# Performance work log

Measured on AMD Instinct MI355X. Metric: run time of the kernel, lower is better.

Reference implementation:

```python
import jax, jax.numpy as jnp
import numpy as np

GROUP = 32
HEADS = 8
EPS = 1e-5


def setup_inputs() -> dict:
    key = jax.random.key(0)
    k1, k2, k3 = jax.random.split(key, 3)
    C = 512
    x = jax.random.normal(k1, (8, C, 32, 32), dtype=jnp.float32)
    gn_w = jnp.ones((C,), dtype=jnp.float32)
    gn_b = jnp.zeros((C,), dtype=jnp.float32)
    # 1x1 convs == channel matmuls; init like torch conv default (kaiming-ish scale)
    w_qkv = jax.random.normal(k2, (3 * C, C), dtype=jnp.float32) * (1.0 / np.sqrt(C))
    w_proj = jax.random.normal(k3, (C, C), dtype=jnp.float32) * (1.0 / np.sqrt(C))
    return {"x": x, "gn_w": gn_w, "gn_b": gn_b, "w_qkv": w_qkv, "w_proj": w_proj}


def _forward(x, gn_w, gn_b, w_qkv, w_proj):
    B, C, H, W = x.shape
    N = H * W
    d = C // HEADS
    scale = d ** -0.5
    # GroupNorm over (channels_per_group, H, W)
    xg = x.reshape(B, GROUP, C // GROUP, H, W)
    mean = xg.mean(axis=(2, 3, 4), keepdims=True)
    var = xg.var(axis=(2, 3, 4), keepdims=True)
    xn = ((xg - mean) * jax.lax.rsqrt(var + EPS)).reshape(B, C, H, W)
    xn = xn * gn_w[None, :, None, None] + gn_b[None, :, None, None]
    # 1x1 conv QKV: [3C, C] x [B, C, H, W]
    qkv = jnp.einsum('oc,bchw->bohw', w_qkv, xn)
    q, k, v = jnp.split(qkv, 3, axis=1)

    def to_heads(t):  # b (h d) H W -> b h N d
        return t.reshape(B, HEADS, d, N).transpose(0, 1, 3, 2)

    q, k, v = to_heads(q), to_heads(k), to_heads(v)
    scores = jnp.einsum('bhid,bhjd->bhij', q, k) * scale
    probs = jax.nn.softmax(scores, axis=-1)
    out = jnp.einsum('bhij,bhjd->bhid', probs, v)
    # b h N d -> b (h d) H W
    out = out.transpose(0, 1, 3, 2).reshape(B, C, H, W)
    out = jnp.einsum('oc,bchw->bohw', w_proj, out)
    return x + out


def reference(x, gn_w, gn_b, w_qkv, w_proj):
    return _forward(x, gn_w, gn_b, w_qkv, w_proj)
```

## Files before the change

kernel.cpp:

```cpp
#include <hip/hip_runtime.h>

typedef __attribute__((ext_vector_type(4))) float f32x4;
typedef __attribute__((ext_vector_type(8))) __bf16 bf16x8;
typedef __attribute__((ext_vector_type(8))) unsigned short ushort8;

#define BATCH 8
#define CH    512
#define NN    1024
#define GRP   32
#define NHEAD 8
#define DH    64
#define QBLK  128
#define KBLK  64

static constexpr size_t OFF_STATS = 0;
static constexpr size_t OFF_WQB   = 4096;
static constexpr size_t OFF_WPB   = OFF_WQB + (size_t)1536*512*2;
static constexpr size_t OFF_XNT   = OFF_WPB + (size_t)512*512*2;
static constexpr size_t OFF_QKB   = OFF_XNT + (size_t)BATCH*NN*CH*2;
static constexpr size_t OFF_VT    = OFF_QKB + (size_t)BATCH*NN*1024*2;
static constexpr size_t OFF_ATTNT = OFF_VT  + (size_t)BATCH*CH*NN*2;

static __device__ __forceinline__ unsigned short f2bf(float f){
  union { float f; unsigned u; } cv; cv.f = f;
  unsigned u = cv.u;
  u += 0x7fffu + ((u >> 16) & 1u);
  return (unsigned short)(u >> 16);
}

static __device__ __forceinline__ unsigned pack2bf(float lo, float hi){
  union { __bf16 h[2]; unsigned u; } v;
  v.h[0] = (__bf16)lo; v.h[1] = (__bf16)hi;
  return v.u;
}

static __device__ __forceinline__ void gload_lds16(const unsigned short* g, unsigned short* l){
  __builtin_amdgcn_global_load_lds((const __attribute__((address_space(1))) void*)g,
                                   (__attribute__((address_space(3))) void*)l, 16, 0, 0);
}

__global__ __launch_bounds__(256) void cvt_w_k(const float* __restrict__ wq, const float* __restrict__ wp,
                                               unsigned short* __restrict__ wqb, unsigned short* __restrict__ wpb){
  int i = blockIdx.x*256 + threadIdx.x;
  if (i < 1536*512) wqb[i] = f2bf(wq[i]);
  if (i < 512*512)  wpb[i] = f2bf(wp[i]);
}

__global__ __launch_bounds__(256) void gn_stats_k(const float* __restrict__ x, float* __restrict__ stats){
  int bg = blockIdx.x;
  const float4* base = (const float4*)(x + (size_t)bg * (16*NN));
  float s = 0.f, ss = 0.f;
  #pragma unroll 4
  for (int idx = threadIdx.x; idx < 16*NN/4; idx += 256){
    float4 v = base[idx];
    s  += (v.x + v.y) + (v.z + v.w);
    ss += (v.x*v.x + v.y*v.y) + (v.z*v.z + v.w*v.w);
  }
  for (int off = 32; off > 0; off >>= 1){ s += __shfl_down(s, off); ss += __shfl_down(ss, off); }
  __shared__ float red[8];
  int w = threadIdx.x >> 6, l = threadIdx.x & 63;
  if (l == 0){ red[w*2] = s; red[w*2+1] = ss; }
  __syncthreads();
  if (threadIdx.x == 0){
    float S  = red[0]+red[2]+red[4]+red[6];
    float SS = red[1]+red[3]+red[5]+red[7];
    float mean = S * (1.f/(16*NN));
    float var  = SS * (1.f/(16*NN)) - mean*mean;
    stats[bg*2]   = mean;
    stats[bg*2+1] = rsqrtf(var + 1e-5f);
  }
}

__global__ __launch_bounds__(256) void gn_apply_k(const float* __restrict__ x, const float* __restrict__ stats,
                                                  const float* __restrict__ gw, const float* __restrict__ gb,
                                                  unsigned short* __restrict__ xnT){
  int b = blockIdx.z, c0 = blockIdx.y*64, n0 = blockIdx.x*64;
  __shared__ unsigned short T[64][65];
  int t = threadIdx.x;
  int nl = t & 63;
  int cb = t >> 6;
  #pragma unroll
  for (int r = 0; r < 16; ++r){
    int cl = cb + r*4;
    int c  = c0 + cl;
    float xv   = x[((size_t)b*CH + c)*NN + n0 + nl];
    float mean = stats[(b*GRP + (c>>4))*2];
    float rstd = stats[(b*GRP + (c>>4))*2 + 1];
    float sc   = rstd * gw[c];
    T[cl][nl]  = f2bf((xv - mean)*sc + gb[c]);
  }
  __syncthreads();
  #pragma unroll
  for (int r = 0; r < 16; ++r){
    int nlocal = cb + r*4;
    xnT[((size_t)b*NN + n0 + nlocal)*CH + c0 + nl] = T[nl][nlocal];
  }
}

__global__ __launch_bounds__(256) void qkv_gemm_k(const unsigned short* __restrict__ wq,
                                                  const unsigned short* __restrict__ xnT,
                                                  unsigned short* __restrict__ qkb,
                                                  unsigned short* __restrict__ vT){
  int b  = blockIdx.z;
  int m0 = blockIdx.y * 128;
  int n0 = blockIdx.x * 128;
  __shared__ unsigned short As[128][64];
  __shared__ unsigned short Bs[128][64];
  int t = threadIdx.x;
  int w = t >> 6, l = t & 63;
  int wm = w >> 1, wn = w & 1;
  f32x4 acc[4][4] = {};
  const unsigned short* Ag = wq  + (size_t)(m0 + w*32)*512;
  const unsigned short* Bg = xnT + ((size_t)b*NN + n0 + w*32)*512;
  int r8 = l >> 3;
  int c8 = ((l & 7) ^ r8) * 8;
  int lr = l & 15, lg = l >> 4;
  int xr = (lr & 7) << 3;
  for (int k0 = 0; k0 < 512; k0 += 64){
    #pragma unroll
    for (int i = 0; i < 4; ++i){
      gload_lds16(Ag + (size_t)(i*8 + r8)*512 + k0 + c8, &As[w*32 + i*8][0]);
      gload_lds16(Bg + (size_t)(i*8 + r8)*512 + k0 + c8, &Bs[w*32 + i*8][0]);
    }
    __syncthreads();
    #pragma unroll
    for (int ks = 0; ks < 2; ++ks){
      bf16x8 af[4], bfr[4];
      #pragma unroll
      for (int mf = 0; mf < 4; ++mf) af[mf]  = *(const bf16x8*)&As[wm*64 + mf*16 + lr][(ks*32 + lg*8) ^ xr];
      #pragma unroll
      for (int nf = 0; nf < 4; ++nf) bfr[nf] = *(const bf16x8*)&Bs[wn*64 + nf*16 + lr][(ks*32 + lg*8) ^ xr];
      #pragma unroll
      for (int mf = 0; mf < 4; ++mf)
        #pragma unroll
        for (int nf = 0; nf < 4; ++nf)
          acc[mf][nf] = __builtin_amdgcn_mfma_f32_16x16x32_bf16(af[mf], bfr[nf], acc[mf][nf], 0, 0, 0);
    }
    __syncthreads();
  }
  int lq = l >> 4;
  float scl = (m0 < 512) ? 0.18033688f : 1.0f;
  if (m0 < 1024){
    #pragma unroll
    for (int mf = 0; mf < 4; ++mf)
      #pragma unroll
      for (int nf = 0; nf < 4; ++nf)
        #pragma unroll
        for (int r = 0; r < 4; ++r){
          int o = m0 + wm*64 + mf*16 + lq*4 + r;
          int n = n0 + wn*64 + nf*16 + lr;
          qkb[((size_t)b*NN + n)*1024 + o] = f2bf(acc[mf][nf][r] * scl);
        }
  } else {
    #pragma unroll
    for (int mf = 0; mf < 4; ++mf)
      #pragma unroll
      for (int nf = 0; nf < 4; ++nf)
        #pragma unroll
        for (int r = 0; r < 4; ++r){
          int o = m0 + wm*64 + mf*16 + lq*4 + r;
          int n = n0 + wn*64 + nf*16 + lr;
          vT[((size_t)b*512 + (o - 1024))*NN + n] = f2bf(acc[mf][nf][r]);
        }
  }
}

#define STAGE_KV(TT, BUF)                                                                \
  {                                                                                      \
    int jj = (TT) * KBLK;                                                                \
    _Pragma("unroll") for (int ch = 0; ch < 2; ++ch){                                    \
      gload_lds16(Kg + (size_t)(jj + w*16 + ch*8 + srow)*1024 + scol,                    \
                  &KV[0][BUF][w*16 + ch*8][0]);                                          \
      gload_lds16(Vg + (size_t)(w*16 + ch*8 + srow)*NN + jj + scol,                      \
                  &KV[1][BUF][w*16 + ch*8][0]);                                          \
    }                                                                                    \
  }

__global__ __launch_bounds__(256) void attn_k(const unsigned short* __restrict__ qkb,
                                              const unsigned short* __restrict__ vT,
                                              unsigned short* __restrict__ attnT){
  int bh = blockIdx.x;
  int b = bh >> 3, h = bh & 7;
  int q0 = blockIdx.y * QBLK;
  int t = threadIdx.x;
  int w = t >> 6, l = t & 63;
  int lr = l & 15, lg = l >> 4;

  __shared__ unsigned short KV[2][2][64][64];

  int srow = l >> 3;
  int scol = ((l & 7) ^ srow) * 8;
  const unsigned short* Kg = qkb + (size_t)b*NN*1024 + 512 + h*DH;
  const unsigned short* Vg = vT  + (size_t)(b*NHEAD + h)*DH*NN;

  bf16x8 qf[2][2];
  #pragma unroll
  for (int mf = 0; mf < 2; ++mf)
    #pragma unroll
    for (int ks = 0; ks < 2; ++ks){
      int row = q0 + w*32 + mf*16 + lr;
      qf[mf][ks] = *(const bf16x8*)(qkb + ((size_t)b*NN + row)*1024 + h*DH + ks*32 + lg*8);
    }

  float lsum[2] = {0.f, 0.f};
  f32x4 accO[2][4] = {};

  STAGE_KV(0, 0)
  __syncthreads();

  for (int tt = 0; tt < 16; ++tt){
    int cur = tt & 1;
    if (tt < 15) STAGE_KV(tt + 1, cur ^ 1)
    int xr = (lr & 7) * 8;
    bf16x8 kf[2][4], vf[2][4];
    #pragma unroll
    for (int ks = 0; ks < 2; ++ks)
      #pragma unroll
      for (int nf = 0; nf < 4; ++nf){
        kf[ks][nf] = *(const bf16x8*)&KV[0][cur][nf*16 + lr][(ks*32 + lg*8) ^ xr];
        vf[ks][nf] = *(const bf16x8*)&KV[1][cur][nf*16 + lr][(ks*32 + lg*8) ^ xr];
      }
    #pragma unroll
    for (int mf = 0; mf < 2; ++mf){
      f32x4 sT[4] = {};
      __builtin_amdgcn_s_setprio(1);
      #pragma unroll
      for (int ks = 0; ks < 2; ++ks)
        #pragma unroll
        for (int nf = 0; nf < 4; ++nf)
          sT[nf] = __builtin_amdgcn_mfma_f32_16x16x32_bf16(kf[ks][nf], qf[mf][ks], sT[nf], 0, 0, 0);
      __builtin_amdgcn_s_setprio(0);
      unsigned pk[4][2];
      #pragma unroll
      for (int nf = 0; nf < 4; ++nf){
        float p0 = exp2f(sT[nf][0]), p1 = exp2f(sT[nf][1]);
        float p2 = exp2f(sT[nf][2]), p3 = exp2f(sT[nf][3]);
        lsum[mf] += (p0 + p1) + (p2 + p3);
        pk[nf][0] = pack2bf(p0, p1);
        pk[nf][1] = pack2bf(p2, p3);
      }
      int srcA = lr + ((lg & 1) << 5);
      int srcB = srcA + 16;
      bool hsel = (lg >> 1) != 0;
      #pragma unroll
      for (int ks = 0; ks < 2; ++ks){
        unsigned a0 = (unsigned)__shfl((int)pk[2*ks  ][0], srcA);
        unsigned a1 = (unsigned)__shfl((int)pk[2*ks  ][1], srcA);
        unsigned a2 = (unsigned)__shfl((int)pk[2*ks  ][0], srcB);
        unsigned a3 = (unsigned)__shfl((int)pk[2*ks  ][1], srcB);
        unsigned b0 = (unsigned)__shfl((int)pk[2*ks+1][0], srcA);
        unsigned b1 = (unsigned)__shfl((int)pk[2*ks+1][1], srcA);
        unsigned b2 = (unsigned)__shfl((int)pk[2*ks+1][0], srcB);
        unsigned b3 = (unsigned)__shfl((int)pk[2*ks+1][1], srcB);
        union { unsigned u[4]; bf16x8 v; } pf;
        pf.u[0] = hsel ? b0 : a0;
        pf.u[1] = hsel ? b1 : a1;
        pf.u[2] = hsel ? b2 : a2;
        pf.u[3] = hsel ? b3 : a3;
        __builtin_amdgcn_s_setprio(1);
        #pragma unroll
        for (int nf = 0; nf < 4; ++nf)
          accO[mf][nf] = __builtin_amdgcn_mfma_f32_16x16x32_bf16(vf[ks][nf], pf.v, accO[mf][nf], 0, 0, 0);
        __builtin_amdgcn_s_setprio(0);
      }
    }
    __syncthreads();
  }

  #pragma unroll
  for (int mf = 0; mf < 2; ++mf){
    lsum[mf] += __shfl_xor(lsum[mf], 16);
    lsum[mf] += __shfl_xor(lsum[mf], 32);
    lsum[mf] = 1.f / lsum[mf];
  }

  unsigned short* Ob = &KV[0][0][0][0] + w * 2304;
  #pragma unroll
  for (int mf = 0; mf < 2; ++mf)
    #pragma unroll
    for (int nf = 0; nf < 4; ++nf)
      #pragma unroll
      for (int r = 0; r < 4; ++r){
        __bf16 hv = (__bf16)(accO[mf][nf][r] * lsum[mf]);
        Ob[mf*1152 + lr*72 + nf*16 + lg*4 + r] = *(unsigned short*)&hv;
      }
  __syncthreads();
  int qr = l >> 2, cc = (l & 3) * 16;
  #pragma unroll
  for (int mf = 0; mf < 2; ++mf){
    bf16x8 o0 = *(const bf16x8*)&Ob[mf*1152 + qr*72 + cc];
    bf16x8 o1 = *(const bf16x8*)&Ob[mf*1152 + qr*72 + cc + 8];
    unsigned short* dst = attnT + ((size_t)b*NN + q0 + w*32 + mf*16 + qr)*CH + h*DH + cc;
    *(bf16x8*)dst = o0;
    *(bf16x8*)(dst + 8) = o1;
  }
}

__global__ __launch_bounds__(256) void proj_gemm_k(const unsigned short* __restrict__ wp,
                                                   const unsigned short* __restrict__ attnT,
                                                   const float* __restrict__ x, float* __restrict__ out){
  int b  = blockIdx.z;
  int m0 = blockIdx.y * 64;
  int n0 = blockIdx.x * 128;
  __shared__ unsigned short As[64][64];
  __shared__ unsigned short Bs[128][64];
  int t = threadIdx.x;
  int w = t >> 6, l = t & 63;
  int wm = w >> 1, wn = w & 1;
  f32x4 acc[2][4] = {};
  const unsigned short* Ag = wp    + (size_t)(m0 + w*16)*512;
  const unsigned short* Bg = attnT + ((size_t)b*NN + n0 + w*32)*512;
  int r8 = l >> 3;
  int c8 = ((l & 7) ^ r8) * 8;
  int lr = l & 15, lg = l >> 4;
  int xr = (lr & 7) << 3;
  for (int k0 = 0; k0 < 512; k0 += 64){
    #pragma unroll
    for (int i = 0; i < 2; ++i)
      gload_lds16(Ag + (size_t)(i*8 + r8)*512 + k0 + c8, &As[w*16 + i*8][0]);
    #pragma unroll
    for (int i = 0; i < 4; ++i)
      gload_lds16(Bg + (size_t)(i*8 + r8)*512 + k0 + c8, &Bs[w*32 + i*8][0]);
    __syncthreads();
    #pragma unroll
    for (int ks = 0; ks < 2; ++ks){
      bf16x8 af[2], bfr[4];
      #pragma unroll
      for (int mf = 0; mf < 2; ++mf) af[mf]  = *(const bf16x8*)&As[wm*32 + mf*16 + lr][(ks*32 + lg*8) ^ xr];
      #pragma unroll
      for (int nf = 0; nf < 4; ++nf) bfr[nf] = *(const bf16x8*)&Bs[wn*64 + nf*16 + lr][(ks*32 + lg*8) ^ xr];
      #pragma unroll
      for (int mf = 0; mf < 2; ++mf)
        #pragma unroll
        for (int nf = 0; nf < 4; ++nf)
          acc[mf][nf] = __builtin_amdgcn_mfma_f32_16x16x32_bf16(af[mf], bfr[nf], acc[mf][nf], 0, 0, 0);
    }
    __syncthreads();
  }
  int lq = l >> 4;
  #pragma unroll
  for (int mf = 0; mf < 2; ++mf)
    #pragma unroll
    for (int nf = 0; nf < 4; ++nf)
      #pragma unroll
      for (int r = 0; r < 4; ++r){
        int o = m0 + wm*32 + mf*16 + lq*4 + r;
        int n = n0 + wn*64 + nf*16 + lr;
        size_t idx = ((size_t)b*CH + o)*NN + n;
        out[idx] = x[idx] + acc[mf][nf][r];
      }
}

extern "C" void kernel_launch(void* const* d_in, const int* in_sizes, int n_in,
                              void* d_out, int out_size, void* d_ws, size_t ws_size,
                              hipStream_t stream){
  const float* x  = (const float*)d_in[0];
  const float* gw = (const float*)d_in[1];
  const float* gb = (const float*)d_in[2];
  const float* wq = (const float*)d_in[3];
  const float* wp = (const float*)d_in[4];
  float* out = (float*)d_out;
  char* ws = (char*)d_ws;
  float*          stats = (float*)(ws + OFF_STATS);
  unsigned short* wqb   = (unsigned short*)(ws + OFF_WQB);
  unsigned short* wpb   = (unsigned short*)(ws + OFF_WPB);
  unsigned short* xnT   = (unsigned short*)(ws + OFF_XNT);
  unsigned short* qkb   = (unsigned short*)(ws + OFF_QKB);
  unsigned short* vT    = (unsigned short*)(ws + OFF_VT);
  unsigned short* attnT = (unsigned short*)(ws + OFF_ATTNT);

  hipLaunchKernelGGL(cvt_w_k,    dim3(3072),      dim3(256), 0, stream, wq, wp, wqb, wpb);
  hipLaunchKernelGGL(gn_stats_k, dim3(256),       dim3(256), 0, stream, x, stats);
  hipLaunchKernelGGL(gn_apply_k, dim3(16, 8, 8),  dim3(256), 0, stream, x, stats, gw, gb, xnT);
  hipLaunchKernelGGL(qkv_gemm_k, dim3(8, 12, 8),  dim3(256), 0, stream, wqb, xnT, qkb, vT);
  hipLaunchKernelGGL(attn_k,     dim3(64, 8),     dim3(256), 0, stream, qkb, vT, attnT);
  hipLaunchKernelGGL(proj_gemm_k,dim3(8, 8, 8),   dim3(256), 0, stream, wpb, attnT, x, out);
}
```

Before: 155.7 us.

## Halve attention query block to double grid and merge prep kernels

```diff
diff --git a/kernel.cpp b/kernel.cpp
--- a/kernel.cpp
+++ b/kernel.cpp
@@ -10,7 +10,7 @@
 #define GRP   32
 #define NHEAD 8
 #define DH    64
-#define QBLK  128
+#define QBLK  64
 #define KBLK  64
 
 static constexpr size_t OFF_STATS = 0;
@@ -39,35 +39,38 @@
                                    (__attribute__((address_space(3))) void*)l, 16, 0, 0);
 }
 
-__global__ __launch_bounds__(256) void cvt_w_k(const float* __restrict__ wq, const float* __restrict__ wp,
-                                               unsigned short* __restrict__ wqb, unsigned short* __restrict__ wpb){
-  int i = blockIdx.x*256 + threadIdx.x;
-  if (i < 1536*512) wqb[i] = f2bf(wq[i]);
-  if (i < 512*512)  wpb[i] = f2bf(wp[i]);
-}
-
-__global__ __launch_bounds__(256) void gn_stats_k(const float* __restrict__ x, float* __restrict__ stats){
-  int bg = blockIdx.x;
-  const float4* base = (const float4*)(x + (size_t)bg * (16*NN));
-  float s = 0.f, ss = 0.f;
-  #pragma unroll 4
-  for (int idx = threadIdx.x; idx < 16*NN/4; idx += 256){
-    float4 v = base[idx];
-    s  += (v.x + v.y) + (v.z + v.w);
-    ss += (v.x*v.x + v.y*v.y) + (v.z*v.z + v.w*v.w);
-  }
-  for (int off = 32; off > 0; off >>= 1){ s += __shfl_down(s, off); ss += __shfl_down(ss, off); }
-  __shared__ float red[8];
-  int w = threadIdx.x >> 6, l = threadIdx.x & 63;
-  if (l == 0){ red[w*2] = s; red[w*2+1] = ss; }
-  __syncthreads();
-  if (threadIdx.x == 0){
-    float S  = red[0]+red[2]+red[4]+red[6];
-    float SS = red[1]+red[3]+red[5]+red[7];
-    float mean = S * (1.f/(16*NN));
-    float var  = SS * (1.f/(16*NN)) - mean*mean;
-    stats[bg*2]   = mean;
-    stats[bg*2+1] = rsqrtf(var + 1e-5f);
+__global__ __launch_bounds__(256) void pre_k(const float* __restrict__ x,
+                                             const float* __restrict__ wq, const float* __restrict__ wp,
+                                             float* __restrict__ stats,
+                                             unsigned short* __restrict__ wqb, unsigned short* __restrict__ wpb){
+  int bid = blockIdx.x;
+  if (bid < 256){
+    int bg = bid;
+    const float4* base = (const float4*)(x + (size_t)bg * (16*NN));
+    float s = 0.f, ss = 0.f;
+    #pragma unroll 4
+    for (int idx = threadIdx.x; idx < 16*NN/4; idx += 256){
+      float4 v = base[idx];
+      s  += (v.x + v.y) + (v.z + v.w);
+      ss += (v.x*v.x + v.y*v.y) + (v.z*v.z + v.w*v.w);
+    }
+    for (int off = 32; off > 0; off >>= 1){ s += __shfl_down(s, off); ss += __shfl_down(ss, off); }
+    __shared__ float red[8];
+    int w = threadIdx.x >> 6, l = threadIdx.x & 63;
+    if (l == 0){ red[w*2] = s; red[w*2+1] = ss; }
+    __syncthreads();
+    if (threadIdx.x == 0){
+      float S  = red[0]+red[2]+red[4]+red[6];
+      float SS = red[1]+red[3]+red[5]+red[7];
+      float mean = S * (1.f/(16*NN));
+      float var  = SS * (1.f/(16*NN)) - mean*mean;
+      stats[bg*2]   = mean;
+      stats[bg*2+1] = rsqrtf(var + 1e-5f);
+    }
+  } else {
+    int i = (bid - 256)*256 + threadIdx.x;
+    if (i < 1536*512) wqb[i] = f2bf(wq[i]);
+    if (i < 512*512)  wpb[i] = f2bf(wp[i]);
   }
 }
 
@@ -193,25 +196,27 @@
   const unsigned short* Kg = qkb + (size_t)b*NN*1024 + 512 + h*DH;
   const unsigned short* Vg = vT  + (size_t)(b*NHEAD + h)*DH*NN;
 
-  bf16x8 qf[2][2];
-  #pragma unroll
-  for (int mf = 0; mf < 2; ++mf)
-    #pragma unroll
-    for (int ks = 0; ks < 2; ++ks){
-      int row = q0 + w*32 + mf*16 + lr;
-      qf[mf][ks] = *(const bf16x8*)(qkb + ((size_t)b*NN + row)*1024 + h*DH + ks*32 + lg*8);
-    }
-
-  float lsum[2] = {0.f, 0.f};
-  f32x4 accO[2][4] = {};
+  bf16x8 qf[2];
+  #pragma unroll
+  for (int ks = 0; ks < 2; ++ks){
+    int row = q0 + w*16 + lr;
+    qf[ks] = *(const bf16x8*)(qkb + ((size_t)b*NN + row)*1024 + h*DH + ks*32 + lg*8);
+  }
+
+  float lsum = 0.f;
+  f32x4 accO[4] = {};
 
   STAGE_KV(0, 0)
   __syncthreads();
+
+  int xr = (lr & 7) * 8;
+  int srcA = lr + ((lg & 1) << 5);
+  int srcB = srcA + 16;
+  bool hsel = (lg >> 1) != 0;
 
   for (int tt = 0; tt < 16; ++tt){
     int cur = tt & 1;
     if (tt < 15) STAGE_KV(tt + 1, cur ^ 1)
-    int xr = (lr & 7) * 8;
     bf16x8 kf[2][4], vf[2][4];
     #pragma unroll
     for (int ks = 0; ks < 2; ++ks)
@@ -220,80 +225,66 @@
         kf[ks][nf] = *(const bf16x8*)&KV[0][cur][nf*16 + lr][(ks*32 + lg*8) ^ xr];
         vf[ks][nf] = *(const bf16x8*)&KV[1][cur][nf*16 + lr][(ks*32 + lg*8) ^ xr];
       }
-    #pragma unroll
-    for (int mf = 0; mf < 2; ++mf){
-      f32x4 sT[4] = {};
+    f32x4 sT[4] = {};
+    __builtin_amdgcn_s_setprio(1);
+    #pragma unroll
+    for (int ks = 0; ks < 2; ++ks)
+      #pragma unroll
+      for (int nf = 0; nf < 4; ++nf)
+        sT[nf] = __builtin_amdgcn_mfma_f32_16x16x32_bf16(kf[ks][nf], qf[ks], sT[nf], 0, 0, 0);
+    __builtin_amdgcn_s_setprio(0);
+    unsigned pk[4][2];
+    #pragma unroll
+    for (int nf = 0; nf < 4; ++nf){
+      float p0 = exp2f(sT[nf][0]), p1 = exp2f(sT[nf][1]);
+      float p2 = exp2f(sT[nf][2]), p3 = exp2f(sT[nf][3]);
+      lsum += (p0 + p1) + (p2 + p3);
+      pk[nf][0] = pack2bf(p0, p1);
+      pk[nf][1] = pack2bf(p2, p3);
+    }
+    #pragma unroll
+    for (int ks = 0; ks < 2; ++ks){
+      unsigned a0 = (unsigned)__shfl((int)pk[2*ks  ][0], srcA);
+      unsigned a1 = (unsigned)__shfl((int)pk[2*ks  ][1], srcA);
+      unsigned a2 = (unsigned)__shfl((int)pk[2*ks  ][0], srcB);
+      unsigned a3 = (unsigned)__shfl((int)pk[2*ks  ][1], srcB);
+      unsigned b0 = (unsigned)__shfl((int)pk[2*ks+1][0], srcA);
+      unsigned b1 = (unsigned)__shfl((int)pk[2*ks+1][1], srcA);
+      unsigned b2 = (unsigned)__shfl((int)pk[2*ks+1][0], srcB);
+      unsigned b3 = (unsigned)__shfl((int)pk[2*ks+1][1], srcB);
+      union { unsigned u[4]; bf16x8 v; } pf;
+      pf.u[0] = hsel ? b0 : a0;
+      pf.u[1] = hsel ? b1 : a1;
+      pf.u[2] = hsel ? b2 : a2;
+      pf.u[3] = hsel ? b3 : a3;
       __builtin_amdgcn_s_setprio(1);
       #pragma unroll
-      for (int ks = 0; ks < 2; ++ks)
-        #pragma unroll
-        for (int nf = 0; nf < 4; ++nf)
-          sT[nf] = __builtin_amdgcn_mfma_f32_16x16x32_bf16(kf[ks][nf], qf[mf][ks], sT[nf], 0, 0, 0);
+      for (int nf = 0; nf < 4; ++nf)
+        accO[nf] = __builtin_amdgcn_mfma_f32_16x16x32_bf16(vf[ks][nf], pf.v, accO[nf], 0, 0, 0);
       __builtin_amdgcn_s_setprio(0);
-      unsigned pk[4][2];
-      #pragma unroll
-      for (int nf = 0; nf < 4; ++nf){
-        float p0 = exp2f(sT[nf][0]), p1 = exp2f(sT[nf][1]);
-        float p2 = exp2f(sT[nf][2]), p3 = exp2f(sT[nf][3]);
-        lsum[mf] += (p0 + p1) + (p2 + p3);
-        pk[nf][0] = pack2bf(p0, p1);
-        pk[nf][1] = pack2bf(p2, p3);
-      }
-      int srcA = lr + ((lg & 1) << 5);
-      int srcB = srcA + 16;
-      bool hsel = (lg >> 1) != 0;
-      #pragma unroll
-      for (int ks = 0; ks < 2; ++ks){
-        unsigned a0 = (unsigned)__shfl((int)pk[2*ks  ][0], srcA);
-        unsigned a1 = (unsigned)__shfl((int)pk[2*ks  ][1], srcA);
-        unsigned a2 = (unsigned)__shfl((int)pk[2*ks  ][0], srcB);
-        unsigned a3 = (unsigned)__shfl((int)pk[2*ks  ][1], srcB);
-        unsigned b0 = (unsigned)__shfl((int)pk[2*ks+1][0], srcA);
-        unsigned b1 = (unsigned)__shfl((int)pk[2*ks+1][1], srcA);
-        unsigned b2 = (unsigned)__shfl((int)pk[2*ks+1][0], srcB);
-        unsigned b3 = (unsigned)__shfl((int)pk[2*ks+1][1], srcB);
-        union { unsigned u[4]; bf16x8 v; } pf;
-        pf.u[0] = hsel ? b0 : a0;
-        pf.u[1] = hsel ? b1 : a1;
-        pf.u[2] = hsel ? b2 : a2;
-        pf.u[3] = hsel ? b3 : a3;
-        __builtin_amdgcn_s_setprio(1);
-        #pragma unroll
-        for (int nf = 0; nf < 4; ++nf)
-          accO[mf][nf] = __builtin_amdgcn_mfma_f32_16x16x32_bf16(vf[ks][nf], pf.v, accO[mf][nf], 0, 0, 0);
-        __builtin_amdgcn_s_setprio(0);
-      }
-    }
-    __syncthreads();
-  }
-
-  #pragma unroll
-  for (int mf = 0; mf < 2; ++mf){
-    lsum[mf] += __shfl_xor(lsum[mf], 16);
-    lsum[mf] += __shfl_xor(lsum[mf], 32);
-    lsum[mf] = 1.f / lsum[mf];
-  }
-
-  unsigned short* Ob = &KV[0][0][0][0] + w * 2304;
-  #pragma unroll
-  for (int mf = 0; mf < 2; ++mf)
-    #pragma unroll
-    for (int nf = 0; nf < 4; ++nf)
-      #pragma unroll
-      for (int r = 0; r < 4; ++r){
-        __bf16 hv = (__bf16)(accO[mf][nf][r] * lsum[mf]);
-        Ob[mf*1152 + lr*72 + nf*16 + lg*4 + r] = *(unsigned short*)&hv;
-      }
+    }
+    __syncthreads();
+  }
+
+  lsum += __shfl_xor(lsum, 16);
+  lsum += __shfl_xor(lsum, 32);
+  lsum = 1.f / lsum;
+
+  unsigned short* Ob = &KV[0][0][0][0] + w * 1152;
+  #pragma unroll
+  for (int nf = 0; nf < 4; ++nf)
+    #pragma unroll
+    for (int r = 0; r < 4; ++r){
+      __bf16 hv = (__bf16)(accO[nf][r] * lsum);
+      Ob[lr*72 + nf*16 + lg*4 + r] = *(unsigned short*)&hv;
+    }
   __syncthreads();
   int qr = l >> 2, cc = (l & 3) * 16;
-  #pragma unroll
-  for (int mf = 0; mf < 2; ++mf){
-    bf16x8 o0 = *(const bf16x8*)&Ob[mf*1152 + qr*72 + cc];
-    bf16x8 o1 = *(const bf16x8*)&Ob[mf*1152 + qr*72 + cc + 8];
-    unsigned short* dst = attnT + ((size_t)b*NN + q0 + w*32 + mf*16 + qr)*CH + h*DH + cc;
-    *(bf16x8*)dst = o0;
-    *(bf16x8*)(dst + 8) = o1;
-  }
+  bf16x8 o0 = *(const bf16x8*)&Ob[qr*72 + cc];
+  bf16x8 o1 = *(const bf16x8*)&Ob[qr*72 + cc + 8];
+  unsigned short* dst = attnT + ((size_t)b*NN + q0 + w*16 + qr)*CH + h*DH + cc;
+  *(bf16x8*)dst = o0;
+  *(bf16x8*)(dst + 8) = o1;
 }
 
 __global__ __launch_bounds__(256) void proj_gemm_k(const unsigned short* __restrict__ wp,
@@ -369,10 +360,9 @@
   unsigned short* vT    = (unsigned short*)(ws + OFF_VT);
   unsigned short* attnT = (unsigned short*)(ws + OFF_ATTNT);
 
-  hipLaunchKernelGGL(cvt_w_k,    dim3(3072),      dim3(256), 0, stream, wq, wp, wqb, wpb);
-  hipLaunchKernelGGL(gn_stats_k, dim3(256),       dim3(256), 0, stream, x, stats);
+  hipLaunchKernelGGL(pre_k,      dim3(3328),      dim3(256), 0, stream, x, wq, wp, stats, wqb, wpb);
   hipLaunchKernelGGL(gn_apply_k, dim3(16, 8, 8),  dim3(256), 0, stream, x, stats, gw, gb, xnT);
   hipLaunchKernelGGL(qkv_gemm_k, dim3(8, 12, 8),  dim3(256), 0, stream, wqb, xnT, qkb, vT);
-  hipLaunchKernelGGL(attn_k,     dim3(64, 8),     dim3(256), 0, stream, qkb, vT, attnT);
+  hipLaunchKernelGGL(attn_k,     dim3(64, 16),    dim3(256), 0, stream, qkb, vT, attnT);
   hipLaunchKernelGGL(proj_gemm_k,dim3(8, 8, 8),   dim3(256), 0, stream, wpb, attnT, x, out);
 }
```

Result: no change. 154.7 us (-0.6%).
